# Optimization experiments

Hardware: AMD Instinct MI355X
Metric: run time of the kernel (lower is better)

## Reference

```python
import jax, jax.numpy as jnp
from jax import lax
import numpy as np

N = 10000      # num_nodes
T = 24         # hist_len
IN_DIM = 16
HID = 128
HEADS = 4
E = 160000     # num_edges
PRED = 24
NEG_SLOPE = 0.2  # GATv2 LeakyReLU default


def _lstm_layer(xs, wih, whh, bih, bhh):
    # xs: [T, N, D]; PyTorch gate order i, f, g, o
    Hh = whh.shape[1]
    h0 = jnp.zeros((xs.shape[1], Hh), xs.dtype)
    def step(carry, xt):
        h, c = carry
        g = xt @ wih.T + bih + h @ whh.T + bhh
        i, f, gg, o = jnp.split(g, 4, axis=-1)
        c = jax.nn.sigmoid(f) * c + jax.nn.sigmoid(i) * jnp.tanh(gg)
        h = jax.nn.sigmoid(o) * jnp.tanh(c)
        return (h, c), h
    (_, _), out = lax.scan(step, (h0, h0), xs)
    return out  # [T, N, Hh]


def _gatv2(z, src, dst, wl, bl, wr, br, att, bias):
    # PyG GATv2Conv: share_weights=False, concat=True, add_self_loops=False
    n = z.shape[0]
    xl = (z @ wl.T + bl).reshape(n, HEADS, HID)   # source/message transform
    xr = (z @ wr.T + br).reshape(n, HEADS, HID)   # target transform
    e = jax.nn.leaky_relu(xl[src] + xr[dst], NEG_SLOPE)   # [E, H, C]
    score = jnp.einsum('ehc,hc->eh', e, att)              # [E, H]
    smax = jax.ops.segment_max(score, dst, num_segments=n)
    p = jnp.exp(score - smax[dst])
    denom = jax.ops.segment_sum(p, dst, num_segments=n)
    alpha = p / (denom[dst] + 1e-16)                      # segment softmax over in-edges
    out = jax.ops.segment_sum(xl[src] * alpha[:, :, None], dst, num_segments=n)
    return out.reshape(n, HEADS * HID) + bias


def setup_inputs() -> dict:
    key = jax.random.key(0)
    ks = iter(jax.random.split(key, 64))
    def W(shape):
        return jax.random.normal(next(ks), shape, jnp.float32) / np.sqrt(shape[-1])
    inp = {}
    inp['x'] = jax.random.normal(next(ks), (N, T, IN_DIM), jnp.float32)
    inp['edge_index'] = jax.random.randint(next(ks), (2, E), 0, N, jnp.int32)
    inp['mlp_in_w0'] = W((HID, IN_DIM)); inp['mlp_in_b0'] = jnp.zeros((HID,), jnp.float32)
    inp['mlp_in_w1'] = W((HID, HID));    inp['mlp_in_b1'] = jnp.zeros((HID,), jnp.float32)
    for l in range(2):  # nn.LSTM(num_layers = lstm_num_layers*2 = 2)
        inp[f'lstm_wih{l}'] = W((4 * HID, HID))
        inp[f'lstm_whh{l}'] = W((4 * HID, HID))
        inp[f'lstm_bih{l}'] = jnp.zeros((4 * HID,), jnp.float32)
        inp[f'lstm_bhh{l}'] = jnp.zeros((4 * HID,), jnp.float32)
    for l in range(2):  # nGAT_layer = 2
        inp[f'gat{l}_wl'] = W((HEADS * HID, HID))
        inp[f'gat{l}_bl'] = jnp.zeros((HEADS * HID,), jnp.float32)
        inp[f'gat{l}_wr'] = W((HEADS * HID, HID))
        inp[f'gat{l}_br'] = jnp.zeros((HEADS * HID,), jnp.float32)
        inp[f'gat{l}_att'] = W((HEADS, HID))
        inp[f'gat{l}_bias'] = jnp.zeros((HEADS * HID,), jnp.float32)
        inp[f'gat{l}_pw'] = W((HID, HEADS * HID))
        inp[f'gat{l}_pb'] = jnp.zeros((HID,), jnp.float32)
    inp['mlp_out_w0'] = W((HID, HID));  inp['mlp_out_b0'] = jnp.zeros((HID,), jnp.float32)
    inp['mlp_out_w1'] = W((PRED, HID)); inp['mlp_out_b1'] = jnp.zeros((PRED,), jnp.float32)
    return inp


def _forward(x, edge_index, mlp_in_w0, mlp_in_b0, mlp_in_w1, mlp_in_b1,
             lstm_wih0, lstm_whh0, lstm_bih0, lstm_bhh0,
             lstm_wih1, lstm_whh1, lstm_bih1, lstm_bhh1,
             gat0_wl, gat0_bl, gat0_wr, gat0_br, gat0_att, gat0_bias, gat0_pw, gat0_pb,
             gat1_wl, gat1_bl, gat1_wr, gat1_br, gat1_att, gat1_bias, gat1_pw, gat1_pb,
             mlp_out_w0, mlp_out_b0, mlp_out_w1, mlp_out_b1):
    src, dst = edge_index[0], edge_index[1]
    h = jnp.transpose(x, (1, 0, 2))                       # [T, N, in_dim]
    # MLP_layers_in: Linear(in,hid), Linear(hid,hid), ReLU
    h = h @ mlp_in_w0.T + mlp_in_b0
    h = jax.nn.relu(h @ mlp_in_w1.T + mlp_in_b1)
    # 2-layer unidirectional LSTM
    h = _lstm_layer(h, lstm_wih0, lstm_whh0, lstm_bih0, lstm_bhh0)
    h = _lstm_layer(h, lstm_wih1, lstm_whh1, lstm_bih1, lstm_bhh1)
    z = h[-1]                                             # [N, HID] last timestep
    # GAT block x2: GATv2Conv -> Linear(heads*hid, hid) -> ReLU
    z = _gatv2(z, src, dst, gat0_wl, gat0_bl, gat0_wr, gat0_br, gat0_att, gat0_bias)
    z = jax.nn.relu(z @ gat0_pw.T + gat0_pb)
    z = _gatv2(z, src, dst, gat1_wl, gat1_bl, gat1_wr, gat1_br, gat1_att, gat1_bias)
    z = jax.nn.relu(z @ gat1_pw.T + gat1_pb)
    # MLP_layers_out: Linear(hid,hid), ReLU, Linear(hid, pred_len)
    z = jax.nn.relu(z @ mlp_out_w0.T + mlp_out_b0)
    return z @ mlp_out_w1.T + mlp_out_b1                  # [N, PRED]


def reference(x, edge_index, mlp_in_w0, mlp_in_b0, mlp_in_w1, mlp_in_b1,
              lstm_wih0, lstm_whh0, lstm_bih0, lstm_bhh0,
              lstm_wih1, lstm_whh1, lstm_bih1, lstm_bhh1,
              gat0_wl, gat0_bl, gat0_wr, gat0_br, gat0_att, gat0_bias, gat0_pw, gat0_pb,
              gat1_wl, gat1_bl, gat1_wr, gat1_br, gat1_att, gat1_bias, gat1_pw, gat1_pb,
              mlp_out_w0, mlp_out_b0, mlp_out_w1, mlp_out_b1):
    return _forward(x, edge_index, mlp_in_w0, mlp_in_b0, mlp_in_w1, mlp_in_b1,
                    lstm_wih0, lstm_whh0, lstm_bih0, lstm_bhh0,
                    lstm_wih1, lstm_whh1, lstm_bih1, lstm_bhh1,
                    gat0_wl, gat0_bl, gat0_wr, gat0_br, gat0_att, gat0_bias, gat0_pw, gat0_pb,
                    gat1_wl, gat1_bl, gat1_wr, gat1_br, gat1_att, gat1_bias, gat1_pw, gat1_pb,
                    mlp_out_w0, mlp_out_b0, mlp_out_w1, mlp_out_b1)
```

## Files before the change

kernel.cpp:

```cpp
#include <hip/hip_runtime.h>
#include <hip/hip_bf16.h>

#define NNODES 10000
#define TLEN 24
#define INDIM 16
#define HID 128
#define GDIM 512

typedef __hip_bfloat16 bf16;
typedef short v8s __attribute__((ext_vector_type(8)));
typedef float v4f __attribute__((ext_vector_type(4)));

__device__ inline float u2f(unsigned u){ return __uint_as_float(u); }

__device__ inline void unpack8(uint4 v, float* f){
  f[0]=u2f(v.x<<16); f[1]=u2f(v.x&0xFFFF0000u);
  f[2]=u2f(v.y<<16); f[3]=u2f(v.y&0xFFFF0000u);
  f[4]=u2f(v.z<<16); f[5]=u2f(v.z&0xFFFF0000u);
  f[6]=u2f(v.w<<16); f[7]=u2f(v.w&0xFFFF0000u);
}

__device__ inline float fsig(float x){
  return __builtin_amdgcn_rcpf(1.f + __expf(-x));
}
__device__ inline float ftanh(float x){
  float t = __expf(-2.f*fabsf(x));
  float r = (1.f - t) * __builtin_amdgcn_rcpf(1.f + t);
  return copysignf(r, x);
}

__global__ __launch_bounds__(256) void conv_w_k(
    const float* s0, const float* s1, const float* s2, const float* s3,
    const float* s4, const float* s5, const float* s6, const float* s7,
    const float* s8, const float* s9, const float* s10,
    bf16* __restrict__ dst, int* __restrict__ deg)
{
  int idx = blockIdx.x*256 + threadIdx.x;
  if (idx < NNODES) deg[idx] = 0;
  if (idx >= 671744) return;
  int c = idx >> 16;
  float v;
  if (c < 10){
    const float* srcs[10] = {s0,s1,s2,s3,s4,s5,s6,s7,s8,s9};
    v = srcs[c][idx & 0xFFFF];
  } else {
    v = s10[idx - 655360];
  }
  dst[idx] = __float2bfloat16(v);
}

__global__ __launch_bounds__(256) void prep_w_k(
    const float* __restrict__ miw0, const float* __restrict__ mib0,
    const float* __restrict__ miw1, const float* __restrict__ mib1,
    const float* __restrict__ bih0, const float* __restrict__ bhh0,
    const float* __restrict__ bih1, const float* __restrict__ bhh1,
    const float* __restrict__ bl0, const float* __restrict__ br0,
    const float* __restrict__ bl1, const float* __restrict__ br1,
    float* __restrict__ Wp, float* __restrict__ bp,
    float* __restrict__ bsum, float* __restrict__ gblr)
{
  int t = threadIdx.x;
  int b = blockIdx.x;
  if (b < 8){
    int idx = b*256 + t;
    int j = idx >> 4, d = idx & 15;
    float s = 0.f;
    for (int k=0;k<HID;k++) s += miw1[j*HID+k] * miw0[k*INDIM+d];
    Wp[idx] = s;
    return;
  }
  if (t < HID){
    float s = mib1[t];
    for (int k=0;k<HID;k++) s += miw1[t*HID+k] * mib0[k];
    bp[t] = s;
  }
  for (int i = t; i < GDIM; i += 256){
    bsum[i]        = bih0[i] + bhh0[i];
    bsum[GDIM + i] = bih1[i] + bhh1[i];
  }
  for (int i = t; i < GDIM; i += 256){
    gblr[i]          = bl0[i];
    gblr[GDIM + i]   = br0[i];
    gblr[1024 + i]   = bl1[i];
    gblr[1536 + i]   = br1[i];
  }
}

__global__ __launch_bounds__(256) void mlp_in_k(
    const float* __restrict__ x, const float* __restrict__ Wp,
    const float* __restrict__ bp, bf16* __restrict__ X0)
{
  __shared__ __align__(16) float xs[64*16];
  const int tid = threadIdx.x;
  const int m0 = blockIdx.x*64;
  {
    int row = tid >> 2, q = tid & 3;
    int m = m0 + row;
    int t = m / NNODES, n = m - t*NNODES;
    float4 v = *(const float4*)(x + ((size_t)n*TLEN + t)*INDIM + q*4);
    *(float4*)(xs + row*16 + q*4) = v;
  }
  const int j = tid & 127;
  const int half = tid >> 7;
  const float* wr = Wp + j*INDIM;
  float4 w0 = *(const float4*)(wr);
  float4 w1 = *(const float4*)(wr + 4);
  float4 w2 = *(const float4*)(wr + 8);
  float4 w3 = *(const float4*)(wr + 12);
  float bj = bp[j];
  __syncthreads();
  #pragma unroll 4
  for (int mi=0; mi<32; mi++){
    int row = mi*2 + half;
    const float* xr = xs + row*16;
    float4 a0 = *(const float4*)(xr);
    float4 a1 = *(const float4*)(xr + 4);
    float4 a2 = *(const float4*)(xr + 8);
    float4 a3 = *(const float4*)(xr + 12);
    float s = bj
      + a0.x*w0.x + a0.y*w0.y + a0.z*w0.z + a0.w*w0.w
      + a1.x*w1.x + a1.y*w1.y + a1.z*w1.z + a1.w*w1.w
      + a2.x*w2.x + a2.y*w2.y + a2.z*w2.z + a2.w*w2.w
      + a3.x*w3.x + a3.y*w3.y + a3.z*w3.z + a3.w*w3.w;
    s = s > 0.f ? s : 0.f;
    X0[(size_t)(m0+row)*HID + j] = __float2bfloat16(s);
  }
}

template<int WRITE_ALL>
__global__ __launch_bounds__(512) void lstm_half(
    const bf16* __restrict__ Xin, const bf16* __restrict__ Wih,
    const bf16* __restrict__ Whh, const float* __restrict__ bias,
    bf16* __restrict__ out)
{
  __shared__ __align__(16) bf16 hsA[16*136];
  __shared__ __align__(16) bf16 hsB[16*136];
  const int tid = threadIdx.x;
  const int lane = tid & 63, w = tid >> 6;
  const int r16 = lane & 15, quad = lane >> 4;
  const int m0 = blockIdx.x*16;

  v8s wbi[4][4], wbh[4][4];
  #pragma unroll
  for (int g=0; g<4; g++)
    #pragma unroll
    for (int kc=0; kc<4; kc++){
      size_t o = (size_t)(g*HID + w*16 + r16)*HID + kc*32 + quad*8;
      wbi[g][kc] = *(const v8s*)(Wih + o);
      wbh[g][kc] = *(const v8s*)(Whh + o);
    }
  float bg[4];
  #pragma unroll
  for (int g=0; g<4; g++) bg[g] = bias[g*HID + w*16 + r16];

  const size_t rowoff = (size_t)(m0 + r16) * HID;

  float c[4];
  #pragma unroll
  for (int i=0;i<4;i++) c[i] = 0.f;

  for (int i = tid; i < 272; i += 512){
    *(uint4*)((char*)hsA + i*16) = make_uint4(0,0,0,0);
    *(uint4*)((char*)hsB + i*16) = make_uint4(0,0,0,0);
  }

  v8s ax[4];
  #pragma unroll
  for (int kc=0; kc<4; kc++)
    ax[kc] = *(const v8s*)(Xin + rowoff + kc*32 + quad*8);

  __syncthreads();

  #pragma unroll 1
  for (int t=0; t<TLEN; t++){
    bf16* hrd = (t & 1) ? hsA : hsB;
    bf16* hwr = (t & 1) ? hsB : hsA;

    v4f acc[4];
    #pragma unroll
    for (int g=0;g<4;g++) acc[g] = (v4f)0.f;

    #pragma unroll
    for (int kc=0; kc<4; kc++)
      #pragma unroll
      for (int g=0;g<4;g++)
        acc[g] = __builtin_amdgcn_mfma_f32_16x16x32_bf16(ax[kc], wbi[g][kc], acc[g], 0, 0, 0);

    {
      int tn = t+1 < TLEN ? t+1 : TLEN-1;
      const bf16* Xn = Xin + (size_t)tn*NNODES*HID;
      #pragma unroll
      for (int kc=0; kc<4; kc++)
        ax[kc] = *(const v8s*)(Xn + rowoff + kc*32 + quad*8);
    }

    #pragma unroll
    for (int kc=0; kc<4; kc++){
      v8s av = *(const v8s*)(hrd + r16*136 + kc*32 + quad*8);
      #pragma unroll
      for (int g=0;g<4;g++)
        acc[g] = __builtin_amdgcn_mfma_f32_16x16x32_bf16(av, wbh[g][kc], acc[g], 0, 0, 0);
    }

    #pragma unroll
    for (int r=0;r<4;r++){
      int lrow = quad*4 + r;
      float iv = acc[0][r] + bg[0];
      float fv = acc[1][r] + bg[1];
      float gv = acc[2][r] + bg[2];
      float ov = acc[3][r] + bg[3];
      float ig = fsig(iv), fg = fsig(fv);
      float gg = ftanh(gv), og = fsig(ov);
      float cn = fg*c[r] + ig*gg;
      c[r] = cn;
      hwr[lrow*136 + w*16 + r16] = __float2bfloat16(og*ftanh(cn));
    }
    __syncthreads();

    if (WRITE_ALL){
      bf16* dst = (bf16*)(Xin + (size_t)t*NNODES*HID);
      for (int i = tid; i < 256; i += 512){
        int row = i >> 4, c8 = (i & 15) * 8;
        *(uint4*)(dst + (size_t)(m0+row)*HID + c8) = *(const uint4*)(hwr + row*136 + c8);
      }
    }
  }

  if (!WRITE_ALL){
    const bf16* hfin = ((TLEN-1) & 1) ? hsB : hsA;
    for (int i = tid; i < 256; i += 512){
      int row = i >> 4, c8 = (i & 15) * 8;
      *(uint4*)(out + (size_t)(m0+row)*HID + c8) = *(const uint4*)(hfin + row*136 + c8);
    }
  }
}

template<int ACT>
__global__ __launch_bounds__(256) void gemm_bt(
    const bf16* __restrict__ A, const bf16* __restrict__ B,
    const float* __restrict__ bias, bf16* __restrict__ C,
    int M, int N, int K)
{
  __shared__ __align__(16) bf16 As[128*40];
  __shared__ __align__(16) bf16 Bs[128*40];
  const int tid = threadIdx.x;
  const int m0 = blockIdx.x*128, n0 = blockIdx.y*128;
  const int lane = tid & 63, wave = tid >> 6;
  const int r16 = lane & 15, quad = lane >> 4;

  v4f acc[2][8];
  #pragma unroll
  for (int a=0;a<2;a++)
    #pragma unroll
    for (int b=0;b<8;b++) acc[a][b] = (v4f)0.f;

  for (int k0=0; k0<K; k0+=32){
    #pragma unroll
    for (int i=0;i<2;i++){
      int li = tid + i*256;
      int row = li >> 2, q4 = li & 3;
      uint4 va = make_uint4(0,0,0,0);
      int gm = m0 + row;
      if (gm < M) va = *(const uint4*)(A + (size_t)gm*K + k0 + q4*8);
      *(uint4*)(As + row*40 + q4*8) = va;
      uint4 vb = make_uint4(0,0,0,0);
      int gn = n0 + row;
      if (gn < N) vb = *(const uint4*)(B + (size_t)gn*K + k0 + q4*8);
      *(uint4*)(Bs + row*40 + q4*8) = vb;
    }
    __syncthreads();
    v8s av[2], bv[8];
    #pragma unroll
    for (int mi=0;mi<2;mi++)
      av[mi] = *(const v8s*)(As + (wave*32 + mi*16 + r16)*40 + quad*8);
    #pragma unroll
    for (int ni=0;ni<8;ni++)
      bv[ni] = *(const v8s*)(Bs + (ni*16 + r16)*40 + quad*8);
    #pragma unroll
    for (int mi=0;mi<2;mi++)
      #pragma unroll
      for (int ni=0;ni<8;ni++)
        acc[mi][ni] = __builtin_amdgcn_mfma_f32_16x16x32_bf16(av[mi], bv[ni], acc[mi][ni], 0, 0, 0);
    __syncthreads();
  }

  #pragma unroll
  for (int mi=0;mi<2;mi++){
    #pragma unroll
    for (int r=0;r<4;r++){
      int row = m0 + wave*32 + mi*16 + quad*4 + r;
      if (row >= M) continue;
      #pragma unroll
      for (int ni=0;ni<8;ni++){
        int col = n0 + ni*16 + r16;
        float v = acc[mi][ni][r] + bias[col];
        if (ACT == 1) v = v > 0.f ? v : 0.f;
        C[(size_t)row*N + col] = __float2bfloat16(v);
      }
    }
  }
}

template<int ACT>
__global__ __launch_bounds__(256) void gemm_bt64(
    const bf16* __restrict__ A, const bf16* __restrict__ B,
    const float* __restrict__ bias, bf16* __restrict__ C,
    int M, int K)
{
  __shared__ __align__(16) bf16 As[64*40];
  __shared__ __align__(16) bf16 Bs[128*40];
  const int tid = threadIdx.x;
  const int m0 = blockIdx.x*64;
  const int lane = tid & 63, wave = tid >> 6;
  const int r16 = lane & 15, quad = lane >> 4;

  v4f acc[8];
  #pragma unroll
  for (int b=0;b<8;b++) acc[b] = (v4f)0.f;

  for (int k0=0; k0<K; k0+=32){
    {
      int row = tid >> 2, q4 = tid & 3;
      uint4 va = make_uint4(0,0,0,0);
      int gm = m0 + row;
      if (gm < M) va = *(const uint4*)(A + (size_t)gm*K + k0 + q4*8);
      *(uint4*)(As + row*40 + q4*8) = va;
    }
    #pragma unroll
    for (int i=0;i<2;i++){
      int li = tid + i*256;
      int row = li >> 2, q4 = li & 3;
      uint4 vb = *(const uint4*)(B + (size_t)row*K + k0 + q4*8);
      *(uint4*)(Bs + row*40 + q4*8) = vb;
    }
    __syncthreads();
    v8s av, bv[8];
    av = *(const v8s*)(As + (wave*16 + r16)*40 + quad*8);
    #pragma unroll
    for (int ni=0;ni<8;ni++)
      bv[ni] = *(const v8s*)(Bs + (ni*16 + r16)*40 + quad*8);
    #pragma unroll
    for (int ni=0;ni<8;ni++)
      acc[ni] = __builtin_amdgcn_mfma_f32_16x16x32_bf16(av, bv[ni], acc[ni], 0, 0, 0);
    __syncthreads();
  }

  #pragma unroll
  for (int r=0;r<4;r++){
    int row = m0 + wave*16 + quad*4 + r;
    if (row >= M) continue;
    #pragma unroll
    for (int ni=0;ni<8;ni++){
      int col = ni*16 + r16;
      float v = acc[ni][r] + bias[col];
      if (ACT == 1) v = v > 0.f ? v : 0.f;
      C[(size_t)row*HID + col] = __float2bfloat16(v);
    }
  }
}

__global__ __launch_bounds__(256) void mlp_out_fused_k(
    const bf16* __restrict__ A, const bf16* __restrict__ B,
    const float* __restrict__ bias, const float* __restrict__ w1,
    const float* __restrict__ b1, float* __restrict__ out, int M)
{
  __shared__ __align__(16) bf16 As[64*40];
  __shared__ __align__(16) bf16 Bs[128*40];
  __shared__ __align__(16) bf16 o0s[64*136];
  const int tid = threadIdx.x;
  const int m0 = blockIdx.x*64;
  const int lane = tid & 63, wave = tid >> 6;
  const int r16 = lane & 15, quad = lane >> 4;

  v4f acc[8];
  #pragma unroll
  for (int b=0;b<8;b++) acc[b] = (v4f)0.f;

  for (int k0=0; k0<HID; k0+=32){
    {
      int row = tid >> 2, q4 = tid & 3;
      uint4 va = make_uint4(0,0,0,0);
      int gm = m0 + row;
      if (gm < M) va = *(const uint4*)(A + (size_t)gm*HID + k0 + q4*8);
      *(uint4*)(As + row*40 + q4*8) = va;
    }
    #pragma unroll
    for (int i=0;i<2;i++){
      int li = tid + i*256;
      int row = li >> 2, q4 = li & 3;
      uint4 vb = *(const uint4*)(B + (size_t)row*HID + k0 + q4*8);
      *(uint4*)(Bs + row*40 + q4*8) = vb;
    }
    __syncthreads();
    v8s av, bv[8];
    av = *(const v8s*)(As + (wave*16 + r16)*40 + quad*8);
    #pragma unroll
    for (int ni=0;ni<8;ni++)
      bv[ni] = *(const v8s*)(Bs + (ni*16 + r16)*40 + quad*8);
    #pragma unroll
    for (int ni=0;ni<8;ni++)
      acc[ni] = __builtin_amdgcn_mfma_f32_16x16x32_bf16(av, bv[ni], acc[ni], 0, 0, 0);
    __syncthreads();
  }

  #pragma unroll
  for (int r=0;r<4;r++){
    int row = wave*16 + quad*4 + r;
    #pragma unroll
    for (int ni=0;ni<8;ni++){
      int col = ni*16 + r16;
      float v = acc[ni][r] + bias[col];
      v = v > 0.f ? v : 0.f;
      o0s[row*136 + col] = __float2bfloat16(v);
    }
  }
  __syncthreads();

  for (int idx = tid; idx < 64*24; idx += 256){
    int row = idx / 24, j = idx - row*24;
    if (m0 + row >= M) continue;
    const bf16* ar = o0s + row*136;
    const float* wr = w1 + j*HID;
    float s = b1[j];
    for (int k=0;k<HID;k+=8){
      float fa[8];
      unpack8(*(const uint4*)(ar+k), fa);
      float4 w0 = *(const float4*)(wr + k);
      float4 w1v = *(const float4*)(wr + k + 4);
      s += fa[0]*w0.x + fa[1]*w0.y + fa[2]*w0.z + fa[3]*w0.w
         + fa[4]*w1v.x + fa[5]*w1v.y + fa[6]*w1v.z + fa[7]*w1v.w;
    }
    out[(size_t)(m0+row)*24 + j] = s;
  }
}

__global__ void deg_count_k(const int* __restrict__ dst, int* __restrict__ deg, int E){
  int e = blockIdx.x*256 + threadIdx.x;
  if (e < E){
    unsigned d = (unsigned)dst[e];
    if (d < (unsigned)NNODES) atomicAdd(&deg[d], 1);
  }
}

__global__ void scan_k(const int* __restrict__ deg, int* __restrict__ offs,
                       int* __restrict__ cursor, int n)
{
  __shared__ int part[256];
  __shared__ int base[256];
  int t = threadIdx.x;
  int lo = t*40, hi = lo+40;
  if (lo > n) lo = n;
  if (hi > n) hi = n;
  int s = 0;
  for (int i=lo;i<hi;i++) s += deg[i];
  part[t] = s;
  __syncthreads();
  if (t == 0){
    int run=0;
    for (int i=0;i<256;i++){ base[i]=run; run+=part[i]; }
    offs[n] = run;
  }
  __syncthreads();
  int run = base[t];
  for (int i=lo;i<hi;i++){ offs[i]=run; cursor[i]=run; run += deg[i]; }
}

__global__ void fill_k(const int* __restrict__ src, const int* __restrict__ dst,
                       int* __restrict__ cursor, int* __restrict__ srcs, int E){
  int e = blockIdx.x*256 + threadIdx.x;
  if (e < E){
    unsigned d = (unsigned)dst[e];
    if (d < (unsigned)NNODES){
      int p = atomicAdd(&cursor[d], 1);
      unsigned s = (unsigned)src[e];
      srcs[p] = (s < (unsigned)NNODES) ? (int)s : 0;
    }
  }
}

__global__ __launch_bounds__(256) void gat_onl(
    const int* __restrict__ offs, const int* __restrict__ srcs,
    const bf16* __restrict__ xc, const float* __restrict__ att,
    const float* __restrict__ gbias, bf16* __restrict__ agg)
{
  int d = blockIdx.x*4 + (threadIdx.x >> 6);
  if (d >= NNODES) return;
  int lane = threadIdx.x & 63;
  float fr[8];
  unpack8(*(const uint4*)(xc + (size_t)d*1024 + 512 + lane*8), fr);
  float4 a0 = *(const float4*)(att + lane*8);
  float4 a1 = *(const float4*)(att + lane*8 + 4);
  float fa[8] = {a0.x,a0.y,a0.z,a0.w,a1.x,a1.y,a1.z,a1.w};
  int i0 = offs[d], i1 = offs[d+1];

  float m = -3.4e38f, den = 0.f;
  float acc[8] = {0,0,0,0,0,0,0,0};

  if (i0 < i1){
    uint4 r0 = *(const uint4*)(xc + (size_t)srcs[i0]*1024 + lane*8);
    uint4 r1 = r0;
    if (i0+1 < i1) r1 = *(const uint4*)(xc + (size_t)srcs[i0+1]*1024 + lane*8);
    for (int i=i0; i<i1; i++){
      uint4 r2 = r1;
      if (i+2 < i1) r2 = *(const uint4*)(xc + (size_t)srcs[i+2]*1024 + lane*8);
      float fl[8];
      unpack8(r0, fl);
      float p = 0.f;
      #pragma unroll
      for (int q=0;q<8;q++){
        float v = fl[q] + fr[q];
        v = v > 0.f ? v : 0.2f*v;
        p += v*fa[q];
      }
      p += __shfl_xor(p, 1); p += __shfl_xor(p, 2);
      p += __shfl_xor(p, 4); p += __shfl_xor(p, 8);
      float mn = fmaxf(m, p);
      float corr = __expf(m - mn);
      float w = __expf(p - mn);
      den = den*corr + w;
      #pragma unroll
      for (int q=0;q<8;q++) acc[q] = acc[q]*corr + w*fl[q];
      m = mn;
      r0 = r1; r1 = r2;
    }
  }
  float r = 1.f/(den + 1e-16f);
  float4 b0 = *(const float4*)(gbias + lane*8);
  float4 b1 = *(const float4*)(gbias + lane*8 + 4);
  float fb[8] = {b0.x,b0.y,b0.z,b0.w,b1.x,b1.y,b1.z,b1.w};
  #pragma unroll
  for (int q=0;q<8;q++)
    agg[(size_t)d*GDIM + lane*8 + q] = __float2bfloat16(acc[q]*r + fb[q]);
}


extern "C" void kernel_launch(void* const* d_in, const int* in_sizes, int n_in,
                              void* d_out, int out_size, void* d_ws, size_t ws_size,
                              hipStream_t stream)
{
  const float* x   = (const float*)d_in[0];
  const int*   ei  = (const int*)d_in[1];
  const int E = in_sizes[1] / 2;
  const int* srcp = ei;
  const int* dstp = ei + E;

  const float* miw0 = (const float*)d_in[2];
  const float* mib0 = (const float*)d_in[3];
  const float* miw1 = (const float*)d_in[4];
  const float* mib1 = (const float*)d_in[5];
  const float* wih0 = (const float*)d_in[6];
  const float* whh0 = (const float*)d_in[7];
  const float* bih0 = (const float*)d_in[8];
  const float* bhh0 = (const float*)d_in[9];
  const float* wih1 = (const float*)d_in[10];
  const float* whh1 = (const float*)d_in[11];
  const float* bih1 = (const float*)d_in[12];
  const float* bhh1 = (const float*)d_in[13];
  const float* g_wl[2]   = {(const float*)d_in[14], (const float*)d_in[22]};
  const float* g_bl[2]   = {(const float*)d_in[15], (const float*)d_in[23]};
  const float* g_wr[2]   = {(const float*)d_in[16], (const float*)d_in[24]};
  const float* g_br[2]   = {(const float*)d_in[17], (const float*)d_in[25]};
  const float* g_att[2]  = {(const float*)d_in[18], (const float*)d_in[26]};
  const float* g_bias[2] = {(const float*)d_in[19], (const float*)d_in[27]};
  const float* g_pw[2]   = {(const float*)d_in[20], (const float*)d_in[28]};
  const float* g_pb[2]   = {(const float*)d_in[21], (const float*)d_in[29]};
  const float* mow0 = (const float*)d_in[30];
  const float* mob0 = (const float*)d_in[31];
  const float* mow1 = (const float*)d_in[32];
  const float* mob1 = (const float*)d_in[33];
  (void)n_in; (void)out_size; (void)ws_size;

  char* base = (char*)d_ws;
  size_t off = 0;
  auto carve = [&](size_t n)->char*{
    char* p = base + off;
    off = (off + n + 255) & ~(size_t)255;
    return p;
  };
  char*  X0r = carve((size_t)TLEN*NNODES*HID*2);
  bf16*  zf  = (bf16*)carve((size_t)NNODES*HID*2);
  float* Wp  = (float*)carve(HID*INDIM*4);
  float* bp  = (float*)carve(HID*4);
  float* bsum= (float*)carve(2*GDIM*4);
  float* gblr= (float*)carve(2*1024*4);
  bf16*  wbf = (bf16*)carve((size_t)671744*2);
  int*   offsb = (int*)carve((size_t)(NNODES+1)*4);
  int*   curs  = (int*)carve((size_t)NNODES*4);
  int*   srcs  = (int*)carve((size_t)E*4);
  int*   deg   = (int*)carve((size_t)NNODES*4);
  bf16*  agg   = (bf16*)carve((size_t)NNODES*GDIM*2);

  const bf16* wih0b = wbf + 0;
  const bf16* whh0b = wbf + 65536;
  const bf16* wih1b = wbf + 131072;
  const bf16* whh1b = wbf + 196608;
  const bf16* wlr0b = wbf + 262144;
  const bf16* pw0b  = wbf + 393216;
  const bf16* wlr1b = wbf + 458752;
  const bf16* pw1b  = wbf + 589824;
  const bf16* mow0b = wbf + 655360;
  const bf16* wlrb[2] = {wlr0b, wlr1b};
  const bf16* pwb[2]  = {pw0b, pw1b};

  bf16* X0 = (bf16*)X0r;
  bf16* xc = (bf16*)X0r;
  bf16* z2 = (bf16*)(X0r + 20480000);
  bf16* z3 = (bf16*)(X0r + 23040000);

  conv_w_k<<<2624, 256, 0, stream>>>(wih0, whh0, wih1, whh1,
                                     g_wl[0], g_wr[0], g_pw[0],
                                     g_wl[1], g_wr[1], g_pw[1], mow0, wbf, deg);
  prep_w_k<<<9, 256, 0, stream>>>(miw0, mib0, miw1, mib1,
                                  bih0, bhh0, bih1, bhh1,
                                  g_bl[0], g_br[0], g_bl[1], g_br[1],
                                  Wp, bp, bsum, gblr);

  mlp_in_k<<<(TLEN*NNODES)/64, 256, 0, stream>>>(x, Wp, bp, X0);

  deg_count_k<<<(E+255)/256, 256, 0, stream>>>(dstp, deg, E);
  scan_k<<<1, 256, 0, stream>>>(deg, offsb, curs, NNODES);
  fill_k<<<(E+255)/256, 256, 0, stream>>>(srcp, dstp, curs, srcs, E);

  const int NBL = NNODES / 16;
  lstm_half<1><<<NBL, 512, 0, stream>>>(X0, wih0b, whh0b, bsum, nullptr);
  lstm_half<0><<<NBL, 512, 0, stream>>>(X0, wih1b, whh1b, bsum + GDIM, zf);

  const bf16* zin = zf;
  bf16* zouts[2] = {z2, z3};
  const int NB64 = (NNODES + 63) / 64;
  for (int l=0; l<2; l++){
    gemm_bt<0><<<dim3(79,8), 256, 0, stream>>>(zin, wlrb[l], gblr + l*1024, xc, NNODES, 1024, HID);
    gat_onl<<<(NNODES+3)/4, 256, 0, stream>>>(offsb, srcs, xc, g_att[l], g_bias[l], agg);
    gemm_bt64<1><<<NB64, 256, 0, stream>>>(agg, pwb[l], g_pb[l], zouts[l], NNODES, GDIM);
    zin = zouts[l];
  }

  mlp_out_fused_k<<<NB64, 256, 0, stream>>>(z3, mow0b, mob0, mow1, mob1,
                                            (float*)d_out, NNODES);
}
```

Before: 580.1 us.

## Process 48 nodes per LSTM block with LDS-staged inputs and cheaper tanh

The LSTM kernel now handles 48 node rows per block instead of 16, processing three 16-row tiles per timestep. This reuses the register-resident weight fragments across more rows and cuts the block count and redundant weight loads. The next timestep's input is prefetched into registers and staged through double-buffered shared memory, the tail rows are guarded, and tanh is simplified to a form without abs and copysign. The trade-offs are fewer blocks (about 209), which may underfill the GPU's compute units, and more work serialized per timestep inside each block.

```diff
diff --git a/kernel.cpp b/kernel.cpp
--- a/kernel.cpp
+++ b/kernel.cpp
@@ -24,9 +24,8 @@
   return __builtin_amdgcn_rcpf(1.f + __expf(-x));
 }
 __device__ inline float ftanh(float x){
-  float t = __expf(-2.f*fabsf(x));
-  float r = (1.f - t) * __builtin_amdgcn_rcpf(1.f + t);
-  return copysignf(r, x);
+  float e = __expf(2.f*x);
+  return 1.f - 2.f*__builtin_amdgcn_rcpf(e + 1.f);
 }
 
 __global__ __launch_bounds__(256) void conv_w_k(
@@ -128,17 +127,17 @@
 }
 
 template<int WRITE_ALL>
-__global__ __launch_bounds__(512) void lstm_half(
+__global__ __launch_bounds__(512) void lstm48(
     const bf16* __restrict__ Xin, const bf16* __restrict__ Wih,
     const bf16* __restrict__ Whh, const float* __restrict__ bias,
     bf16* __restrict__ out)
 {
-  __shared__ __align__(16) bf16 hsA[16*136];
-  __shared__ __align__(16) bf16 hsB[16*136];
+  __shared__ __align__(16) bf16 hs[2][48*136];
+  __shared__ __align__(16) bf16 xs[2][48*136];
   const int tid = threadIdx.x;
   const int lane = tid & 63, w = tid >> 6;
   const int r16 = lane & 15, quad = lane >> 4;
-  const int m0 = blockIdx.x*16;
+  const int m0 = blockIdx.x*48;
 
   v8s wbi[4][4], wbh[4][4];
   #pragma unroll
@@ -153,84 +152,109 @@
   #pragma unroll
   for (int g=0; g<4; g++) bg[g] = bias[g*HID + w*16 + r16];
 
-  const size_t rowoff = (size_t)(m0 + r16) * HID;
-
-  float c[4];
-  #pragma unroll
-  for (int i=0;i<4;i++) c[i] = 0.f;
-
-  for (int i = tid; i < 272; i += 512){
-    *(uint4*)((char*)hsA + i*16) = make_uint4(0,0,0,0);
-    *(uint4*)((char*)hsB + i*16) = make_uint4(0,0,0,0);
-  }
-
-  v8s ax[4];
-  #pragma unroll
-  for (int kc=0; kc<4; kc++)
-    ax[kc] = *(const v8s*)(Xin + rowoff + kc*32 + quad*8);
-
+  const int row0 = tid >> 4;
+  const int c8   = (tid & 15) * 8;
+  const int row1 = 32 + (tid >> 4);
+  const int gr0 = m0 + row0;
+  const int gr1 = m0 + row1;
+  const int gr0c = gr0 < NNODES ? gr0 : NNODES-1;
+  const int gr1c = gr1 < NNODES ? gr1 : NNODES-1;
+  const bf16* ldp0 = Xin + (size_t)gr0c*HID + c8;
+  const bf16* ldp1 = Xin + (size_t)gr1c*HID + c8;
+  bf16* stp0 = (bf16*)Xin + (size_t)gr0*HID + c8;
+  bf16* stp1 = (bf16*)Xin + (size_t)gr1*HID + c8;
+  const size_t TS = (size_t)NNODES*HID;
+
+  for (int i = tid; i < 816; i += 512)
+    *(uint4*)((char*)hs[0] + i*16) = make_uint4(0,0,0,0);
+
+  {
+    uint4 a = *(const uint4*)ldp0;
+    *(uint4*)(&xs[0][row0*136 + c8]) = a;
+    if (tid < 256){
+      uint4 b = *(const uint4*)ldp1;
+      *(uint4*)(&xs[0][row1*136 + c8]) = b;
+    }
+  }
   __syncthreads();
+
+  float c[3][4];
+  #pragma unroll
+  for (int tl=0; tl<3; tl++)
+    #pragma unroll
+    for (int r=0; r<4; r++) c[tl][r] = 0.f;
+
+  const int fb = r16*136 + quad*8;
 
   #pragma unroll 1
   for (int t=0; t<TLEN; t++){
-    bf16* hrd = (t & 1) ? hsA : hsB;
-    bf16* hwr = (t & 1) ? hsB : hsA;
-
-    v4f acc[4];
-    #pragma unroll
-    for (int g=0;g<4;g++) acc[g] = (v4f)0.f;
-
-    #pragma unroll
-    for (int kc=0; kc<4; kc++)
-      #pragma unroll
-      for (int g=0;g<4;g++)
-        acc[g] = __builtin_amdgcn_mfma_f32_16x16x32_bf16(ax[kc], wbi[g][kc], acc[g], 0, 0, 0);
-
-    {
-      int tn = t+1 < TLEN ? t+1 : TLEN-1;
-      const bf16* Xn = Xin + (size_t)tn*NNODES*HID;
-      #pragma unroll
-      for (int kc=0; kc<4; kc++)
-        ax[kc] = *(const v8s*)(Xn + rowoff + kc*32 + quad*8);
-    }
-
-    #pragma unroll
-    for (int kc=0; kc<4; kc++){
-      v8s av = *(const v8s*)(hrd + r16*136 + kc*32 + quad*8);
-      #pragma unroll
-      for (int g=0;g<4;g++)
-        acc[g] = __builtin_amdgcn_mfma_f32_16x16x32_bf16(av, wbh[g][kc], acc[g], 0, 0, 0);
-    }
-
-    #pragma unroll
-    for (int r=0;r<4;r++){
-      int lrow = quad*4 + r;
-      float iv = acc[0][r] + bg[0];
-      float fv = acc[1][r] + bg[1];
-      float gv = acc[2][r] + bg[2];
-      float ov = acc[3][r] + bg[3];
-      float ig = fsig(iv), fg = fsig(fv);
-      float gg = ftanh(gv), og = fsig(ov);
-      float cn = fg*c[r] + ig*gg;
-      c[r] = cn;
-      hwr[lrow*136 + w*16 + r16] = __float2bfloat16(og*ftanh(cn));
-    }
+    const int cur = t & 1, nxt = cur ^ 1;
+    const bf16* xrd = xs[cur];
+    const bf16* hrd = hs[cur];
+    bf16* hwr = hs[nxt];
+
+    const int tn = (t+1 < TLEN) ? t+1 : TLEN-1;
+    uint4 xa = *(const uint4*)(ldp0 + (size_t)tn*TS);
+    uint4 xb;
+    if (tid < 256) xb = *(const uint4*)(ldp1 + (size_t)tn*TS);
+
+    #pragma unroll
+    for (int tl=0; tl<3; tl++){
+      v4f acc[4];
+      #pragma unroll
+      for (int g=0; g<4; g++) acc[g] = (v4f)0.f;
+
+      #pragma unroll
+      for (int kc=0; kc<4; kc++){
+        v8s av = *(const v8s*)(xrd + tl*2176 + fb + kc*32);
+        #pragma unroll
+        for (int g=0; g<4; g++)
+          acc[g] = __builtin_amdgcn_mfma_f32_16x16x32_bf16(av, wbi[g][kc], acc[g], 0, 0, 0);
+      }
+      #pragma unroll
+      for (int kc=0; kc<4; kc++){
+        v8s hv = *(const v8s*)(hrd + tl*2176 + fb + kc*32);
+        #pragma unroll
+        for (int g=0; g<4; g++)
+          acc[g] = __builtin_amdgcn_mfma_f32_16x16x32_bf16(hv, wbh[g][kc], acc[g], 0, 0, 0);
+      }
+
+      #pragma unroll
+      for (int r=0; r<4; r++){
+        float iv = acc[0][r] + bg[0];
+        float fv = acc[1][r] + bg[1];
+        float gv = acc[2][r] + bg[2];
+        float ov = acc[3][r] + bg[3];
+        float ig = fsig(iv), fg = fsig(fv);
+        float gg = ftanh(gv), og = fsig(ov);
+        float cn = fg*c[tl][r] + ig*gg;
+        c[tl][r] = cn;
+        hwr[(tl*16 + quad*4 + r)*136 + w*16 + r16] = __float2bfloat16(og*ftanh(cn));
+      }
+    }
+
+    *(uint4*)(&xs[nxt][row0*136 + c8]) = xa;
+    if (tid < 256) *(uint4*)(&xs[nxt][row1*136 + c8]) = xb;
+
     __syncthreads();
 
     if (WRITE_ALL){
-      bf16* dst = (bf16*)(Xin + (size_t)t*NNODES*HID);
-      for (int i = tid; i < 256; i += 512){
-        int row = i >> 4, c8 = (i & 15) * 8;
-        *(uint4*)(dst + (size_t)(m0+row)*HID + c8) = *(const uint4*)(hwr + row*136 + c8);
+      uint4 h0 = *(const uint4*)(&hwr[row0*136 + c8]);
+      if (gr0 < NNODES) *(uint4*)(stp0 + (size_t)t*TS) = h0;
+      if (tid < 256){
+        uint4 h1v = *(const uint4*)(&hwr[row1*136 + c8]);
+        if (gr1 < NNODES) *(uint4*)(stp1 + (size_t)t*TS) = h1v;
       }
     }
   }
 
   if (!WRITE_ALL){
-    const bf16* hfin = ((TLEN-1) & 1) ? hsB : hsA;
-    for (int i = tid; i < 256; i += 512){
-      int row = i >> 4, c8 = (i & 15) * 8;
-      *(uint4*)(out + (size_t)(m0+row)*HID + c8) = *(const uint4*)(hfin + row*136 + c8);
+    const bf16* hf = hs[TLEN & 1];
+    uint4 h0 = *(const uint4*)(&hf[row0*136 + c8]);
+    if (gr0 < NNODES) *(uint4*)(out + (size_t)gr0*HID + c8) = h0;
+    if (tid < 256){
+      uint4 h1v = *(const uint4*)(&hf[row1*136 + c8]);
+      if (gr1 < NNODES) *(uint4*)(out + (size_t)gr1*HID + c8) = h1v;
     }
   }
 }
@@ -621,9 +645,9 @@
   scan_k<<<1, 256, 0, stream>>>(deg, offsb, curs, NNODES);
   fill_k<<<(E+255)/256, 256, 0, stream>>>(srcp, dstp, curs, srcs, E);
 
-  const int NBL = NNODES / 16;
-  lstm_half<1><<<NBL, 512, 0, stream>>>(X0, wih0b, whh0b, bsum, nullptr);
-  lstm_half<0><<<NBL, 512, 0, stream>>>(X0, wih1b, whh1b, bsum + GDIM, zf);
+  const int NBL48 = (NNODES + 47) / 48;
+  lstm48<1><<<NBL48, 512, 0, stream>>>(X0, wih0b, whh0b, bsum, nullptr);
+  lstm48<0><<<NBL48, 512, 0, stream>>>(X0, wih1b, whh1b, bsum + GDIM, zf);
 
   const bf16* zin = zf;
   bf16* zouts[2] = {z2, z3};
```

Result: faster. 526.4 us (-9.3%).

## Restructure LSTM kernel to 48-row tiles with 1024 threads and shared gate buffer

Applied to the files above, without the earlier changes.

Replaces the 16-row, 512-thread LSTM kernel with one that handles 48 node rows per block using 16 waves. Each wave owns 32 gate columns, so the resident weights per wave are halved and reused across three row tiles. Gate pre-activations are staged through a shared float buffer so the nonlinearity runs in a row-per-wave layout. The input for the next step is prefetched into shared memory, and the per-step hidden stores are deferred by one step. The shared-memory footprint is much larger and the grid has far fewer blocks (about 209), which risks poor occupancy and load balance.

```diff
diff --git a/kernel.cpp b/kernel.cpp
--- a/kernel.cpp
+++ b/kernel.cpp
@@ -12,21 +12,13 @@
 typedef float v4f __attribute__((ext_vector_type(4)));
 
 __device__ inline float u2f(unsigned u){ return __uint_as_float(u); }
+__device__ inline float frcp(float x){ return __builtin_amdgcn_rcpf(x); }
 
 __device__ inline void unpack8(uint4 v, float* f){
   f[0]=u2f(v.x<<16); f[1]=u2f(v.x&0xFFFF0000u);
   f[2]=u2f(v.y<<16); f[3]=u2f(v.y&0xFFFF0000u);
   f[4]=u2f(v.z<<16); f[5]=u2f(v.z&0xFFFF0000u);
   f[6]=u2f(v.w<<16); f[7]=u2f(v.w&0xFFFF0000u);
-}
-
-__device__ inline float fsig(float x){
-  return __builtin_amdgcn_rcpf(1.f + __expf(-x));
-}
-__device__ inline float ftanh(float x){
-  float t = __expf(-2.f*fabsf(x));
-  float r = (1.f - t) * __builtin_amdgcn_rcpf(1.f + t);
-  return copysignf(r, x);
 }
 
 __global__ __launch_bounds__(256) void conv_w_k(
@@ -128,110 +120,122 @@
 }
 
 template<int WRITE_ALL>
-__global__ __launch_bounds__(512) void lstm_half(
+__global__ __launch_bounds__(1024) void lstm_cs(
     const bf16* __restrict__ Xin, const bf16* __restrict__ Wih,
     const bf16* __restrict__ Whh, const float* __restrict__ bias,
     bf16* __restrict__ out)
 {
-  __shared__ __align__(16) bf16 hsA[16*136];
-  __shared__ __align__(16) bf16 hsB[16*136];
+  __shared__ __align__(16) float gs[48*516];
+  __shared__ __align__(16) bf16 xs[48*136];
+  __shared__ __align__(16) bf16 hb[48*136];
   const int tid = threadIdx.x;
-  const int lane = tid & 63, w = tid >> 6;
+  const int w = tid >> 6;
+  const int lane = tid & 63;
   const int r16 = lane & 15, quad = lane >> 4;
-  const int m0 = blockIdx.x*16;
-
-  v8s wbi[4][4], wbh[4][4];
-  #pragma unroll
-  for (int g=0; g<4; g++)
+  const int m0 = blockIdx.x*48;
+
+  v8s wbi[2][4], wbh[2][4];
+  #pragma unroll
+  for (int ct=0; ct<2; ct++)
     #pragma unroll
     for (int kc=0; kc<4; kc++){
-      size_t o = (size_t)(g*HID + w*16 + r16)*HID + kc*32 + quad*8;
-      wbi[g][kc] = *(const v8s*)(Wih + o);
-      wbh[g][kc] = *(const v8s*)(Whh + o);
-    }
-  float bg[4];
-  #pragma unroll
-  for (int g=0; g<4; g++) bg[g] = bias[g*HID + w*16 + r16];
-
-  const size_t rowoff = (size_t)(m0 + r16) * HID;
-
-  float c[4];
-  #pragma unroll
-  for (int i=0;i<4;i++) c[i] = 0.f;
-
-  for (int i = tid; i < 272; i += 512){
-    *(uint4*)((char*)hsA + i*16) = make_uint4(0,0,0,0);
-    *(uint4*)((char*)hsB + i*16) = make_uint4(0,0,0,0);
-  }
-
-  v8s ax[4];
-  #pragma unroll
-  for (int kc=0; kc<4; kc++)
-    ax[kc] = *(const v8s*)(Xin + rowoff + kc*32 + quad*8);
-
+      size_t o = (size_t)(w*32 + ct*16 + r16)*HID + kc*32 + quad*8;
+      wbi[ct][kc] = *(const v8s*)(Wih + o);
+      wbh[ct][kc] = *(const v8s*)(Whh + o);
+    }
+  const float bw0 = bias[w*32 + r16];
+  const float bw1 = bias[w*32 + 16 + r16];
+
+  const int srow = tid >> 4;
+  const int c8   = (tid & 15) * 8;
+  const int gr   = m0 + srow;
+  const int grc  = gr < NNODES ? gr : NNODES-1;
+  const size_t TS = (size_t)NNODES*HID;
+  const bf16* ldp = Xin + (size_t)grc*HID + c8;
+  bf16* stp = (bf16*)Xin + (size_t)gr*HID + c8;
+
+  for (int i = tid; i < 816; i += 1024)
+    ((uint4*)hb)[i] = make_uint4(0,0,0,0);
+  if (tid < 768)
+    *(uint4*)(xs + srow*136 + c8) = *(const uint4*)ldp;
   __syncthreads();
+
+  float c[3][2];
+  #pragma unroll
+  for (int rt=0; rt<3; rt++){ c[rt][0] = 0.f; c[rt][1] = 0.f; }
+
+  const int fb = r16*136 + quad*8;
 
   #pragma unroll 1
   for (int t=0; t<TLEN; t++){
-    bf16* hrd = (t & 1) ? hsA : hsB;
-    bf16* hwr = (t & 1) ? hsB : hsA;
-
-    v4f acc[4];
-    #pragma unroll
-    for (int g=0;g<4;g++) acc[g] = (v4f)0.f;
-
-    #pragma unroll
-    for (int kc=0; kc<4; kc++)
-      #pragma unroll
-      for (int g=0;g<4;g++)
-        acc[g] = __builtin_amdgcn_mfma_f32_16x16x32_bf16(ax[kc], wbi[g][kc], acc[g], 0, 0, 0);
-
-    {
+    uint4 xa;
+    if (tid < 768){
       int tn = t+1 < TLEN ? t+1 : TLEN-1;
-      const bf16* Xn = Xin + (size_t)tn*NNODES*HID;
-      #pragma unroll
-      for (int kc=0; kc<4; kc++)
-        ax[kc] = *(const v8s*)(Xn + rowoff + kc*32 + quad*8);
-    }
-
-    #pragma unroll
-    for (int kc=0; kc<4; kc++){
-      v8s av = *(const v8s*)(hrd + r16*136 + kc*32 + quad*8);
-      #pragma unroll
-      for (int g=0;g<4;g++)
-        acc[g] = __builtin_amdgcn_mfma_f32_16x16x32_bf16(av, wbh[g][kc], acc[g], 0, 0, 0);
-    }
-
-    #pragma unroll
-    for (int r=0;r<4;r++){
-      int lrow = quad*4 + r;
-      float iv = acc[0][r] + bg[0];
-      float fv = acc[1][r] + bg[1];
-      float gv = acc[2][r] + bg[2];
-      float ov = acc[3][r] + bg[3];
-      float ig = fsig(iv), fg = fsig(fv);
-      float gg = ftanh(gv), og = fsig(ov);
-      float cn = fg*c[r] + ig*gg;
-      c[r] = cn;
-      hwr[lrow*136 + w*16 + r16] = __float2bfloat16(og*ftanh(cn));
-    }
-    __syncthreads();
-
-    if (WRITE_ALL){
-      bf16* dst = (bf16*)(Xin + (size_t)t*NNODES*HID);
-      for (int i = tid; i < 256; i += 512){
-        int row = i >> 4, c8 = (i & 15) * 8;
-        *(uint4*)(dst + (size_t)(m0+row)*HID + c8) = *(const uint4*)(hwr + row*136 + c8);
+      xa = *(const uint4*)(ldp + (size_t)tn*TS);
+      if (WRITE_ALL && t > 0 && gr < NNODES)
+        *(uint4*)(stp + (size_t)(t-1)*TS) = *(const uint4*)(hb + srow*136 + c8);
+    }
+    #pragma unroll
+    for (int rt=0; rt<3; rt++){
+      v4f a0 = (v4f)0.f, a1 = (v4f)0.f;
+      #pragma unroll
+      for (int kc=0; kc<4; kc++){
+        v8s av = *(const v8s*)(xs + rt*2176 + fb + kc*32);
+        a0 = __builtin_amdgcn_mfma_f32_16x16x32_bf16(av, wbi[0][kc], a0, 0, 0, 0);
+        a1 = __builtin_amdgcn_mfma_f32_16x16x32_bf16(av, wbi[1][kc], a1, 0, 0, 0);
       }
-    }
-  }
-
-  if (!WRITE_ALL){
-    const bf16* hfin = ((TLEN-1) & 1) ? hsB : hsA;
-    for (int i = tid; i < 256; i += 512){
-      int row = i >> 4, c8 = (i & 15) * 8;
-      *(uint4*)(out + (size_t)(m0+row)*HID + c8) = *(const uint4*)(hfin + row*136 + c8);
-    }
+      #pragma unroll
+      for (int kc=0; kc<4; kc++){
+        v8s hv = *(const v8s*)(hb + rt*2176 + fb + kc*32);
+        a0 = __builtin_amdgcn_mfma_f32_16x16x32_bf16(hv, wbh[0][kc], a0, 0, 0, 0);
+        a1 = __builtin_amdgcn_mfma_f32_16x16x32_bf16(hv, wbh[1][kc], a1, 0, 0, 0);
+      }
+      int gwb = (rt*16 + quad*4)*516 + w*32 + r16;
+      #pragma unroll
+      for (int r=0; r<4; r++){
+        gs[gwb + r*516]      = a0[r] + bw0;
+        gs[gwb + r*516 + 16] = a1[r] + bw1;
+      }
+    }
+    __syncthreads();
+    #pragma unroll
+    for (int rt=0; rt<3; rt++){
+      const int erow = rt*16 + w;
+      const float* grd = gs + erow*516 + 2*lane;
+      float2 gi = *(const float2*)(grd);
+      float2 gf = *(const float2*)(grd + 128);
+      float2 gg = *(const float2*)(grd + 256);
+      float2 go = *(const float2*)(grd + 384);
+      unsigned short hu[2];
+      #pragma unroll
+      for (int j=0; j<2; j++){
+        float iv = j ? gi.y : gi.x;
+        float fv = j ? gf.y : gf.x;
+        float gv = j ? gg.y : gg.x;
+        float ov = j ? go.y : go.x;
+        float sf = frcp(1.f + __expf(-fv));
+        float ei = __expf(-iv);
+        float tg = __expf(-2.f*fabsf(gv));
+        float itg = copysignf((1.f - tg)*frcp((1.f + ei)*(1.f + tg)), gv);
+        float cn = sf*c[rt][j] + itg;
+        c[rt][j] = cn;
+        float eo = __expf(-ov);
+        float tc = __expf(-2.f*fabsf(cn));
+        float hh = copysignf((1.f - tc)*frcp((1.f + eo)*(1.f + tc)), cn);
+        __hip_bfloat16 hv16 = __float2bfloat16(hh);
+        hu[j] = *reinterpret_cast<unsigned short*>(&hv16);
+      }
+      *(unsigned*)(hb + erow*136 + 2*lane) = ((unsigned)hu[1] << 16) | hu[0];
+    }
+    if (tid < 768)
+      *(uint4*)(xs + srow*136 + c8) = xa;
+    __syncthreads();
+  }
+
+  if (tid < 768 && gr < NNODES){
+    uint4 h = *(const uint4*)(hb + srow*136 + c8);
+    if (WRITE_ALL) *(uint4*)(stp + (size_t)(TLEN-1)*TS) = h;
+    else           *(uint4*)(out + (size_t)gr*HID + c8) = h;
   }
 }
 
@@ -621,9 +625,9 @@
   scan_k<<<1, 256, 0, stream>>>(deg, offsb, curs, NNODES);
   fill_k<<<(E+255)/256, 256, 0, stream>>>(srcp, dstp, curs, srcs, E);
 
-  const int NBL = NNODES / 16;
-  lstm_half<1><<<NBL, 512, 0, stream>>>(X0, wih0b, whh0b, bsum, nullptr);
-  lstm_half<0><<<NBL, 512, 0, stream>>>(X0, wih1b, whh1b, bsum + GDIM, zf);
+  const int NBL48 = (NNODES + 47) / 48;
+  lstm_cs<1><<<NBL48, 1024, 0, stream>>>(X0, wih0b, whh0b, bsum, nullptr);
+  lstm_cs<0><<<NBL48, 1024, 0, stream>>>(X0, wih1b, whh1b, bsum + GDIM, zf);
 
   const bf16* zin = zf;
   bf16* zouts[2] = {z2, z3};
```

After: 559.8 us. -3.5%, faster.
